# Kernel optimization log

Measured on AMD Instinct MI355X. Metric: run time of the kernel, lower is better.

Reference implementation:

```python
import jax, jax.numpy as jnp
import numpy as np

N_NODES = 50000


def setup_inputs() -> dict:
    key = jax.random.key(0)
    ks = jax.random.split(key, 6)
    L, d = 3, 128
    x = jax.random.normal(ks[0], (N_NODES, d), dtype=jnp.float32)
    edge_index = jax.random.randint(ks[1], (2, 640000), 0, N_NODES, dtype=jnp.int64)
    s = 1.0 / np.sqrt(d)
    W1 = jax.random.normal(ks[2], (L, d, d), dtype=jnp.float32) * s
    W2 = jax.random.normal(ks[3], (L, d, d), dtype=jnp.float32) * s
    b1 = jnp.zeros((L, d), dtype=jnp.float32)
    b2 = jnp.zeros((L, d), dtype=jnp.float32)
    eps = jnp.zeros((L,), dtype=jnp.float32)
    final_w = jax.random.normal(ks[4], (d + L * d, d), dtype=jnp.float32) / np.sqrt(d + L * d)
    final_b = jnp.zeros((d,), dtype=jnp.float32)
    return {"x": x, "edge_index": edge_index, "W1": W1, "b1": b1,
            "W2": W2, "b2": b2, "eps": eps, "final_w": final_w, "final_b": final_b}


def reference(x, edge_index, W1, b1, W2, b2, eps, final_w, final_b):
    src, dst = edge_index[0], edge_index[1]
    num_layers = W1.shape[0]
    xs = [x]
    h = x
    for l in range(num_layers):
        # GINConv: sum-aggregate neighbor features, add (1+eps)*self, then 2-layer MLP
        agg = jax.ops.segment_sum(h[src], dst, num_segments=N_NODES)  # [N, d]
        z = (1.0 + eps[l]) * h + agg
        z = jax.nn.relu(z @ W1[l] + b1[l])
        h = jax.nn.relu(z @ W2[l] + b2[l])
        xs.append(h)
    out = jnp.concatenate(xs, axis=-1)  # [N, in + L*out]
    return out @ final_w + final_b
```

## Files before the change

### kernel.cpp

```cpp
#include <hip/hip_runtime.h>

#define NNODES 50000
#define NEDGES 640000
#define D 128

typedef unsigned short u16;
typedef unsigned int u32;
typedef __bf16 bf16x8 __attribute__((ext_vector_type(8)));
typedef float f32x4 __attribute__((ext_vector_type(4)));
union AB { uint4 u4; bf16x8 f; };

__device__ __forceinline__ u16 f2b(float f) {
    u32 u = __float_as_uint(f);
    return (u16)((u + 0x7fffu + ((u >> 16) & 1u)) >> 16);
}
__device__ __forceinline__ u32 pack2(float lo, float hi) {
    return (u32)f2b(lo) | ((u32)f2b(hi) << 16);
}
__device__ __forceinline__ float blo(u32 v) { return __uint_as_float(v << 16); }
__device__ __forceinline__ float bhi(u32 v) { return __uint_as_float(v & 0xffff0000u); }

__device__ __forceinline__ void acc8(float* a, uint4 v) {
    a[0] += blo(v.x); a[1] += bhi(v.x);
    a[2] += blo(v.y); a[3] += bhi(v.y);
    a[4] += blo(v.z); a[5] += bhi(v.z);
    a[6] += blo(v.w); a[7] += bhi(v.w);
}


__global__ void k_hist(const int* __restrict__ dst, int* __restrict__ cnt) {
    int e = blockIdx.x * 256 + threadIdx.x;
    if (e < NEDGES) atomicAdd(&cnt[dst[e]], 1);
}

__global__ void k_scan1(const int* __restrict__ cnt, int* __restrict__ rp,
                        int* __restrict__ bsum) {
    __shared__ int s[256];
    int tid = threadIdx.x;
    int i = blockIdx.x * 256 + tid;
    int v = (i < NNODES) ? cnt[i] : 0;
    s[tid] = v;
    __syncthreads();
    for (int off = 1; off < 256; off <<= 1) {
        int t = (tid >= off) ? s[tid - off] : 0;
        __syncthreads();
        s[tid] += t;
        __syncthreads();
    }
    if (i < NNODES) rp[i] = s[tid] - v;
    if (tid == 255) bsum[blockIdx.x] = s[255];
}

__global__ void k_scan2(int* __restrict__ bsum, int nb) {
    __shared__ int s[256];
    int tid = threadIdx.x;
    int v = (tid < nb) ? bsum[tid] : 0;
    s[tid] = v;
    __syncthreads();
    for (int off = 1; off < 256; off <<= 1) {
        int t = (tid >= off) ? s[tid - off] : 0;
        __syncthreads();
        s[tid] += t;
        __syncthreads();
    }
    if (tid < nb) bsum[tid] = s[tid] - v;
}

__global__ void k_add(int* __restrict__ rp, const int* __restrict__ bsum) {
    int i = blockIdx.x * 256 + threadIdx.x;
    if (i < NNODES) rp[i] += bsum[blockIdx.x];
    if (i == 0) rp[NNODES] = NEDGES;
}

__global__ void k_scatter(const int* __restrict__ src, const int* __restrict__ dst,
                          const int* __restrict__ rp, int* __restrict__ cnt,
                          int* __restrict__ srcs) {
    int e = blockIdx.x * 256 + threadIdx.x;
    if (e < NEDGES) {
        int dn = dst[e];
        int old = atomicSub(&cnt[dn], 1);
        srcs[rp[dn] + old - 1] = src[e];
    }
}

__global__ void k_prep(const float* __restrict__ W1, const float* __restrict__ W2,
                       const float* __restrict__ fw, const float* __restrict__ x,
                       u16* __restrict__ wT1, u16* __restrict__ wT2,
                       u16* __restrict__ fwTc, u32* __restrict__ xb) {
    int idx = blockIdx.x * 256 + threadIdx.x;
    if (idx < 3 * 16384) {
        int l = idx >> 14, r = idx & 16383, n = r >> 7, k = r & 127;
        wT1[idx] = f2b(W1[l * 16384 + k * 128 + n]);
        wT2[idx] = f2b(W2[l * 16384 + k * 128 + n]);
    }
    if (idx < 4 * 16384) {
        int ch = idx >> 14, r = idx & 16383, n = r >> 7, k = r & 127;
        fwTc[idx] = f2b(fw[(ch * 128 + k) * 128 + n]);
    }
    if (idx < NNODES * 64) {
        float2 v = ((const float2*)x)[idx];
        xb[idx] = pack2(v.x, v.y);
    }
}

__global__ void k_agg(const uint4* __restrict__ h4, const int* __restrict__ rp,
                      const int* __restrict__ srcs, const float* __restrict__ epsp,
                      uint4* __restrict__ z4) {
    int tid = threadIdx.x;
    int c = tid & 15;
    int node = (blockIdx.x * 256 + tid) >> 4;
    int gbase = tid & 48;
    float sc = 1.0f + epsp[0];

    uint4 sv = h4[node * 16 + c];
    float acc[8];
    acc[0] = sc * blo(sv.x); acc[1] = sc * bhi(sv.x);
    acc[2] = sc * blo(sv.y); acc[3] = sc * bhi(sv.y);
    acc[4] = sc * blo(sv.z); acc[5] = sc * bhi(sv.z);
    acc[6] = sc * blo(sv.w); acc[7] = sc * bhi(sv.w);

    int beg = rp[node], end = rp[node + 1];
    for (int base = beg; base < end; base += 16) {
        int n = end - base; if (n > 16) n = 16;
        int myidx = (base + c < end) ? srcs[base + c] : 0;
        int j = 0;
        for (; j + 8 <= n; j += 8) {
            int s0 = __shfl(myidx, gbase + j + 0, 64);
            int s1 = __shfl(myidx, gbase + j + 1, 64);
            int s2 = __shfl(myidx, gbase + j + 2, 64);
            int s3 = __shfl(myidx, gbase + j + 3, 64);
            int s4 = __shfl(myidx, gbase + j + 4, 64);
            int s5 = __shfl(myidx, gbase + j + 5, 64);
            int s6 = __shfl(myidx, gbase + j + 6, 64);
            int s7 = __shfl(myidx, gbase + j + 7, 64);
            uint4 v0 = h4[s0 * 16 + c]; uint4 v1 = h4[s1 * 16 + c];
            uint4 v2 = h4[s2 * 16 + c]; uint4 v3 = h4[s3 * 16 + c];
            uint4 v4 = h4[s4 * 16 + c]; uint4 v5 = h4[s5 * 16 + c];
            uint4 v6 = h4[s6 * 16 + c]; uint4 v7 = h4[s7 * 16 + c];
            acc8(acc, v0); acc8(acc, v1); acc8(acc, v2); acc8(acc, v3);
            acc8(acc, v4); acc8(acc, v5); acc8(acc, v6); acc8(acc, v7);
        }
        for (; j + 4 <= n; j += 4) {
            int s0 = __shfl(myidx, gbase + j + 0, 64);
            int s1 = __shfl(myidx, gbase + j + 1, 64);
            int s2 = __shfl(myidx, gbase + j + 2, 64);
            int s3 = __shfl(myidx, gbase + j + 3, 64);
            uint4 v0 = h4[s0 * 16 + c]; uint4 v1 = h4[s1 * 16 + c];
            uint4 v2 = h4[s2 * 16 + c]; uint4 v3 = h4[s3 * 16 + c];
            acc8(acc, v0); acc8(acc, v1); acc8(acc, v2); acc8(acc, v3);
        }
        for (; j < n; ++j) {
            int s0 = __shfl(myidx, gbase + j, 64);
            uint4 v0 = h4[s0 * 16 + c];
            acc8(acc, v0);
        }
    }

    uint4 o;
    o.x = pack2(acc[0], acc[1]); o.y = pack2(acc[2], acc[3]);
    o.z = pack2(acc[4], acc[5]); o.w = pack2(acc[6], acc[7]);
    z4[node * 16 + c] = o;
}

__launch_bounds__(256, 2)
__global__ void k_mlp(const u16* __restrict__ A, const u16* __restrict__ wT1g,
                      const float* __restrict__ b1, const u16* __restrict__ wT2g,
                      const float* __restrict__ b2, u16* __restrict__ H) {
    __shared__ u16 Tb[128 * 128];
    __shared__ u16 wbuf[128 * 128];
    uint4* Tb4 = (uint4*)Tb;
    uint4* wb4 = (uint4*)wbuf;
    int tid = threadIdx.x;
    int r0 = blockIdx.x * 128;
    int wave = tid >> 6, lane = tid & 63, l16 = lane & 15, quad = lane >> 4;

    {
        const uint4* g = (const uint4*)wT1g;
        for (int i = tid; i < 2048; i += 256) {
            int n = i >> 4, ch = i & 15;
            wb4[n * 16 + ((ch + n) & 15)] = g[i];
        }
    }

    AB a[2][4];
#pragma unroll
    for (int s = 0; s < 2; ++s) {
        int row = r0 + wave * 32 + s * 16 + l16;
#pragma unroll
        for (int kb = 0; kb < 4; ++kb) {
            if (row < NNODES)
                a[s][kb].u4 = *(const uint4*)&A[row * 128 + kb * 32 + quad * 8];
            else
                a[s][kb].u4 = make_uint4(0, 0, 0, 0);
        }
    }
    __syncthreads();

    f32x4 acc[2][8];
#pragma unroll
    for (int col = 0; col < 8; ++col) {
        float bv = b1[col * 16 + l16];
        acc[0][col] = (f32x4){bv, bv, bv, bv};
        acc[1][col] = (f32x4){bv, bv, bv, bv};
    }
#pragma unroll
    for (int col = 0; col < 8; ++col) {
#pragma unroll
        for (int kb = 0; kb < 4; ++kb) {
            AB b;
            int n = col * 16 + l16;
            b.u4 = wb4[n * 16 + ((kb * 4 + quad + n) & 15)];
            acc[0][col] = __builtin_amdgcn_mfma_f32_16x16x32_bf16(a[0][kb].f, b.f, acc[0][col], 0, 0, 0);
            acc[1][col] = __builtin_amdgcn_mfma_f32_16x16x32_bf16(a[1][kb].f, b.f, acc[1][col], 0, 0, 0);
        }
    }

#pragma unroll
    for (int s = 0; s < 2; ++s)
#pragma unroll
        for (int col = 0; col < 8; ++col)
#pragma unroll
            for (int r = 0; r < 4; ++r) {
                int row = wave * 32 + s * 16 + quad * 4 + r;
                int kcol = col * 16 + l16;
                int ch = kcol >> 3;
                Tb[row * 128 + ((ch + row) & 15) * 8 + (kcol & 7)] =
                    f2b(fmaxf(acc[s][col][r], 0.f));
            }
    __syncthreads();

    {
        const uint4* g = (const uint4*)wT2g;
        for (int i = tid; i < 2048; i += 256) {
            int n = i >> 4, ch = i & 15;
            wb4[n * 16 + ((ch + n) & 15)] = g[i];
        }
    }
    AB a2[2][4];
#pragma unroll
    for (int s = 0; s < 2; ++s) {
        int m = wave * 32 + s * 16 + l16;
#pragma unroll
        for (int kb = 0; kb < 4; ++kb)
            a2[s][kb].u4 = Tb4[m * 16 + ((kb * 4 + quad + m) & 15)];
    }
    __syncthreads();

#pragma unroll
    for (int col = 0; col < 8; ++col) {
        float bv = b2[col * 16 + l16];
        acc[0][col] = (f32x4){bv, bv, bv, bv};
        acc[1][col] = (f32x4){bv, bv, bv, bv};
    }
#pragma unroll
    for (int col = 0; col < 8; ++col) {
#pragma unroll
        for (int kb = 0; kb < 4; ++kb) {
            AB b;
            int n = col * 16 + l16;
            b.u4 = wb4[n * 16 + ((kb * 4 + quad + n) & 15)];
            acc[0][col] = __builtin_amdgcn_mfma_f32_16x16x32_bf16(a2[0][kb].f, b.f, acc[0][col], 0, 0, 0);
            acc[1][col] = __builtin_amdgcn_mfma_f32_16x16x32_bf16(a2[1][kb].f, b.f, acc[1][col], 0, 0, 0);
        }
    }
    __syncthreads();

#pragma unroll
    for (int s = 0; s < 2; ++s)
#pragma unroll
        for (int col = 0; col < 8; ++col)
#pragma unroll
            for (int r = 0; r < 4; ++r) {
                int row = wave * 32 + s * 16 + quad * 4 + r;
                int kcol = col * 16 + l16;
                int ch = kcol >> 3;
                Tb[row * 128 + ((ch + row) & 15) * 8 + (kcol & 7)] =
                    f2b(fmaxf(acc[s][col][r], 0.f));
            }
    __syncthreads();

    for (int i = tid; i < 2048; i += 256) {
        int r = i >> 4, ch = i & 15;
        int grow = r0 + r;
        if (grow < NNODES)
            *(uint4*)&H[grow * 128 + ch * 8] = Tb4[r * 16 + ((ch + r) & 15)];
    }
}

__launch_bounds__(256, 2)
__global__ void k_final(const u16* __restrict__ xb, const u16* __restrict__ h1,
                        const u16* __restrict__ h2b, const u16* __restrict__ h3,
                        const u16* __restrict__ fwTc, const float* __restrict__ fb,
                        float* __restrict__ out) {
    __shared__ u16 wbuf[128 * 128];
    uint4* wb4 = (uint4*)wbuf;
    int tid = threadIdx.x;
    int wave = tid >> 6, lane = tid & 63, l16 = lane & 15, quad = lane >> 4;
    int r0 = blockIdx.x * 128 + wave * 32;

    f32x4 acc[2][8];
#pragma unroll
    for (int col = 0; col < 8; ++col) {
        float bv = fb[col * 16 + l16];
        acc[0][col] = (f32x4){bv, bv, bv, bv};
        acc[1][col] = (f32x4){bv, bv, bv, bv};
    }

    const u16* chin[4] = {xb, h1, h2b, h3};
    for (int chn = 0; chn < 4; ++chn) {
        __syncthreads();
        {
            const uint4* g = (const uint4*)(fwTc + chn * 16384);
            for (int i = tid; i < 2048; i += 256) {
                int n = i >> 4, ch = i & 15;
                wb4[n * 16 + ((ch + n) & 15)] = g[i];
            }
        }
        const u16* cp = chin[chn];
        AB a[2][4];
#pragma unroll
        for (int s = 0; s < 2; ++s) {
            int row = r0 + s * 16 + l16;
#pragma unroll
            for (int kb = 0; kb < 4; ++kb) {
                if (row < NNODES)
                    a[s][kb].u4 = *(const uint4*)&cp[row * 128 + kb * 32 + quad * 8];
                else
                    a[s][kb].u4 = make_uint4(0, 0, 0, 0);
            }
        }
        __syncthreads();
#pragma unroll
        for (int col = 0; col < 8; ++col) {
#pragma unroll
            for (int kb = 0; kb < 4; ++kb) {
                AB b;
                int n = col * 16 + l16;
                b.u4 = wb4[n * 16 + ((kb * 4 + quad + n) & 15)];
                acc[0][col] = __builtin_amdgcn_mfma_f32_16x16x32_bf16(a[0][kb].f, b.f, acc[0][col], 0, 0, 0);
                acc[1][col] = __builtin_amdgcn_mfma_f32_16x16x32_bf16(a[1][kb].f, b.f, acc[1][col], 0, 0, 0);
            }
        }
    }

#pragma unroll
    for (int s = 0; s < 2; ++s)
#pragma unroll
        for (int col = 0; col < 8; ++col)
#pragma unroll
            for (int r = 0; r < 4; ++r) {
                int row = r0 + s * 16 + quad * 4 + r;
                if (row < NNODES) out[row * 128 + col * 16 + l16] = acc[s][col][r];
            }
}

extern "C" void kernel_launch(void* const* d_in, const int* in_sizes, int n_in,
                              void* d_out, int out_size, void* d_ws, size_t ws_size,
                              hipStream_t stream) {
    const float* x   = (const float*)d_in[0];
    const int*   ei  = (const int*)d_in[1];
    const float* W1  = (const float*)d_in[2];
    const float* b1  = (const float*)d_in[3];
    const float* W2  = (const float*)d_in[4];
    const float* b2  = (const float*)d_in[5];
    const float* eps = (const float*)d_in[6];
    const float* fw  = (const float*)d_in[7];
    const float* fb  = (const float*)d_in[8];
    float* out = (float*)d_out;

    const int* srcA = ei;
    const int* dstA = ei + NEDGES;

    char* p = (char*)d_ws;
    size_t off = 0;
    auto take = [&](size_t bytes) {
        char* r = p + off;
        off = (off + bytes + 255) & ~(size_t)255;
        return r;
    };
    int* rp   = (int*)take((NNODES + 1) * sizeof(int));
    int* cnt  = (int*)take(NNODES * sizeof(int));
    int* bsum = (int*)take(256 * sizeof(int));
    int* srcs = (int*)take(NEDGES * sizeof(int));
    u16* wT1  = (u16*)take(3 * 16384 * sizeof(u16));
    u16* wT2  = (u16*)take(3 * 16384 * sizeof(u16));
    u16* fwTc = (u16*)take(4 * 16384 * sizeof(u16));
    u16* xb   = (u16*)take((size_t)NNODES * D * sizeof(u16));
    u16* zb   = (u16*)take((size_t)NNODES * D * sizeof(u16));
    u16* hb1  = (u16*)take((size_t)NNODES * D * sizeof(u16));
    u16* hb2  = (u16*)take((size_t)NNODES * D * sizeof(u16));
    u16* hb3  = (u16*)take((size_t)NNODES * D * sizeof(u16));
    (void)ws_size; (void)in_sizes; (void)n_in; (void)out_size;

    hipMemsetAsync(cnt, 0, NNODES * sizeof(int), stream);

    int nb = (NNODES + 255) / 256;
    k_hist<<<(NEDGES + 255) / 256, 256, 0, stream>>>(dstA, cnt);
    k_scan1<<<nb, 256, 0, stream>>>(cnt, rp, bsum);
    k_scan2<<<1, 256, 0, stream>>>(bsum, nb);
    k_add<<<nb, 256, 0, stream>>>(rp, bsum);
    k_scatter<<<(NEDGES + 255) / 256, 256, 0, stream>>>(srcA, dstA, rp, cnt, srcs);
    k_prep<<<(NNODES * 64 + 255) / 256, 256, 0, stream>>>(W1, W2, fw, x, wT1, wT2, fwTc, (u32*)xb);

    const u16* hin = xb;
    u16* houts[3] = {hb1, hb2, hb3};
    int gm = (NNODES + 127) / 128;
    for (int l = 0; l < 3; ++l) {
        k_agg<<<NNODES * 16 / 256, 256, 0, stream>>>((const uint4*)hin, rp, srcs, eps + l, (uint4*)zb);
        k_mlp<<<gm, 256, 0, stream>>>(zb, wT1 + l * 16384, b1 + l * D,
                                      wT2 + l * 16384, b2 + l * D, houts[l]);
        hin = houts[l];
    }
    k_final<<<gm, 256, 0, stream>>>(xb, hb1, hb2, hb3, fwTc, fb, out);
}
```

Baseline: 300.9 us.

## Fuse neighbor aggregation into MLP kernel and fold final projection into last layer

After: 315.8 us. 5.0% more time.

```diff
diff --git a/kernel.cpp b/kernel.cpp
--- a/kernel.cpp
+++ b/kernel.cpp
@@ -103,69 +103,16 @@
     }
 }
 
-__global__ void k_agg(const uint4* __restrict__ h4, const int* __restrict__ rp,
-                      const int* __restrict__ srcs, const float* __restrict__ epsp,
-                      uint4* __restrict__ z4) {
-    int tid = threadIdx.x;
-    int c = tid & 15;
-    int node = (blockIdx.x * 256 + tid) >> 4;
-    int gbase = tid & 48;
-    float sc = 1.0f + epsp[0];
-
-    uint4 sv = h4[node * 16 + c];
-    float acc[8];
-    acc[0] = sc * blo(sv.x); acc[1] = sc * bhi(sv.x);
-    acc[2] = sc * blo(sv.y); acc[3] = sc * bhi(sv.y);
-    acc[4] = sc * blo(sv.z); acc[5] = sc * bhi(sv.z);
-    acc[6] = sc * blo(sv.w); acc[7] = sc * bhi(sv.w);
-
-    int beg = rp[node], end = rp[node + 1];
-    for (int base = beg; base < end; base += 16) {
-        int n = end - base; if (n > 16) n = 16;
-        int myidx = (base + c < end) ? srcs[base + c] : 0;
-        int j = 0;
-        for (; j + 8 <= n; j += 8) {
-            int s0 = __shfl(myidx, gbase + j + 0, 64);
-            int s1 = __shfl(myidx, gbase + j + 1, 64);
-            int s2 = __shfl(myidx, gbase + j + 2, 64);
-            int s3 = __shfl(myidx, gbase + j + 3, 64);
-            int s4 = __shfl(myidx, gbase + j + 4, 64);
-            int s5 = __shfl(myidx, gbase + j + 5, 64);
-            int s6 = __shfl(myidx, gbase + j + 6, 64);
-            int s7 = __shfl(myidx, gbase + j + 7, 64);
-            uint4 v0 = h4[s0 * 16 + c]; uint4 v1 = h4[s1 * 16 + c];
-            uint4 v2 = h4[s2 * 16 + c]; uint4 v3 = h4[s3 * 16 + c];
-            uint4 v4 = h4[s4 * 16 + c]; uint4 v5 = h4[s5 * 16 + c];
-            uint4 v6 = h4[s6 * 16 + c]; uint4 v7 = h4[s7 * 16 + c];
-            acc8(acc, v0); acc8(acc, v1); acc8(acc, v2); acc8(acc, v3);
-            acc8(acc, v4); acc8(acc, v5); acc8(acc, v6); acc8(acc, v7);
-        }
-        for (; j + 4 <= n; j += 4) {
-            int s0 = __shfl(myidx, gbase + j + 0, 64);
-            int s1 = __shfl(myidx, gbase + j + 1, 64);
-            int s2 = __shfl(myidx, gbase + j + 2, 64);
-            int s3 = __shfl(myidx, gbase + j + 3, 64);
-            uint4 v0 = h4[s0 * 16 + c]; uint4 v1 = h4[s1 * 16 + c];
-            uint4 v2 = h4[s2 * 16 + c]; uint4 v3 = h4[s3 * 16 + c];
-            acc8(acc, v0); acc8(acc, v1); acc8(acc, v2); acc8(acc, v3);
-        }
-        for (; j < n; ++j) {
-            int s0 = __shfl(myidx, gbase + j, 64);
-            uint4 v0 = h4[s0 * 16 + c];
-            acc8(acc, v0);
-        }
-    }
-
-    uint4 o;
-    o.x = pack2(acc[0], acc[1]); o.y = pack2(acc[2], acc[3]);
-    o.z = pack2(acc[4], acc[5]); o.w = pack2(acc[6], acc[7]);
-    z4[node * 16 + c] = o;
-}
-
+template <bool FINAL>
 __launch_bounds__(256, 2)
-__global__ void k_mlp(const u16* __restrict__ A, const u16* __restrict__ wT1g,
-                      const float* __restrict__ b1, const u16* __restrict__ wT2g,
-                      const float* __restrict__ b2, u16* __restrict__ H) {
+__global__ void k_layer(const uint4* __restrict__ h4, const int* __restrict__ rp,
+                        const int* __restrict__ srcs, const float* __restrict__ epsp,
+                        const u16* __restrict__ wT1g, const float* __restrict__ b1,
+                        const u16* __restrict__ wT2g, const float* __restrict__ b2,
+                        u16* __restrict__ H,
+                        const u16* __restrict__ xbg, const u16* __restrict__ h1g,
+                        const u16* __restrict__ h2g, const u16* __restrict__ fwTc,
+                        const float* __restrict__ fb, float* __restrict__ out) {
     __shared__ u16 Tb[128 * 128];
     __shared__ u16 wbuf[128 * 128];
     uint4* Tb4 = (uint4*)Tb;
@@ -182,17 +129,73 @@
         }
     }
 
+    {
+        int c = tid & 15;
+        int grp = tid >> 4;
+        int gbase = lane & 48;
+        float sc = 1.0f + epsp[0];
+        for (int p = 0; p < 8; ++p) {
+            int rloc = p * 16 + grp;
+            int node = r0 + rloc;
+            uint4 o = make_uint4(0, 0, 0, 0);
+            if (node < NNODES) {
+                uint4 sv = h4[node * 16 + c];
+                float acc[8];
+                acc[0] = sc * blo(sv.x); acc[1] = sc * bhi(sv.x);
+                acc[2] = sc * blo(sv.y); acc[3] = sc * bhi(sv.y);
+                acc[4] = sc * blo(sv.z); acc[5] = sc * bhi(sv.z);
+                acc[6] = sc * blo(sv.w); acc[7] = sc * bhi(sv.w);
+                int beg = rp[node], end = rp[node + 1];
+                for (int base = beg; base < end; base += 16) {
+                    int n = end - base; if (n > 16) n = 16;
+                    int myidx = (base + c < end) ? srcs[base + c] : 0;
+                    int j = 0;
+                    for (; j + 8 <= n; j += 8) {
+                        int s0 = __shfl(myidx, gbase + j + 0, 64);
+                        int s1 = __shfl(myidx, gbase + j + 1, 64);
+                        int s2 = __shfl(myidx, gbase + j + 2, 64);
+                        int s3 = __shfl(myidx, gbase + j + 3, 64);
+                        int s4 = __shfl(myidx, gbase + j + 4, 64);
+                        int s5 = __shfl(myidx, gbase + j + 5, 64);
+                        int s6 = __shfl(myidx, gbase + j + 6, 64);
+                        int s7 = __shfl(myidx, gbase + j + 7, 64);
+                        uint4 v0 = h4[s0 * 16 + c]; uint4 v1 = h4[s1 * 16 + c];
+                        uint4 v2 = h4[s2 * 16 + c]; uint4 v3 = h4[s3 * 16 + c];
+                        uint4 v4 = h4[s4 * 16 + c]; uint4 v5 = h4[s5 * 16 + c];
+                        uint4 v6 = h4[s6 * 16 + c]; uint4 v7 = h4[s7 * 16 + c];
+                        acc8(acc, v0); acc8(acc, v1); acc8(acc, v2); acc8(acc, v3);
+                        acc8(acc, v4); acc8(acc, v5); acc8(acc, v6); acc8(acc, v7);
+                    }
+                    for (; j + 4 <= n; j += 4) {
+                        int s0 = __shfl(myidx, gbase + j + 0, 64);
+                        int s1 = __shfl(myidx, gbase + j + 1, 64);
+                        int s2 = __shfl(myidx, gbase + j + 2, 64);
+                        int s3 = __shfl(myidx, gbase + j + 3, 64);
+                        uint4 v0 = h4[s0 * 16 + c]; uint4 v1 = h4[s1 * 16 + c];
+                        uint4 v2 = h4[s2 * 16 + c]; uint4 v3 = h4[s3 * 16 + c];
+                        acc8(acc, v0); acc8(acc, v1); acc8(acc, v2); acc8(acc, v3);
+                    }
+                    for (; j < n; ++j) {
+                        int s0 = __shfl(myidx, gbase + j, 64);
+                        uint4 v0 = h4[s0 * 16 + c];
+                        acc8(acc, v0);
+                    }
+                }
+                o.x = pack2(acc[0], acc[1]); o.y = pack2(acc[2], acc[3]);
+                o.z = pack2(acc[4], acc[5]); o.w = pack2(acc[6], acc[7]);
+            }
+            Tb4[rloc * 16 + ((c + rloc) & 15)] = o;
+        }
+    }
+    __syncthreads();
+
     AB a[2][4];
 #pragma unroll
     for (int s = 0; s < 2; ++s) {
-        int row = r0 + wave * 32 + s * 16 + l16;
-#pragma unroll
-        for (int kb = 0; kb < 4; ++kb) {
-            if (row < NNODES)
-                a[s][kb].u4 = *(const uint4*)&A[row * 128 + kb * 32 + quad * 8];
-            else
-                a[s][kb].u4 = make_uint4(0, 0, 0, 0);
-        }
+        int m = wave * 32 + s * 16 + l16;
+#pragma unroll
+        for (int kb = 0; kb < 4; ++kb)
+            a[s][kb].u4 = Tb4[m * 16 + ((kb * 4 + quad + m) & 15)];
     }
     __syncthreads();
 
@@ -263,7 +266,6 @@
             acc[1][col] = __builtin_amdgcn_mfma_f32_16x16x32_bf16(a2[1][kb].f, b.f, acc[1][col], 0, 0, 0);
         }
     }
-    __syncthreads();
 
 #pragma unroll
     for (int s = 0; s < 2; ++s)
@@ -277,81 +279,78 @@
                 Tb[row * 128 + ((ch + row) & 15) * 8 + (kcol & 7)] =
                     f2b(fmaxf(acc[s][col][r], 0.f));
             }
-    __syncthreads();
-
-    for (int i = tid; i < 2048; i += 256) {
-        int r = i >> 4, ch = i & 15;
-        int grow = r0 + r;
-        if (grow < NNODES)
-            *(uint4*)&H[grow * 128 + ch * 8] = Tb4[r * 16 + ((ch + r) & 15)];
-    }
-}
-
-__launch_bounds__(256, 2)
-__global__ void k_final(const u16* __restrict__ xb, const u16* __restrict__ h1,
-                        const u16* __restrict__ h2b, const u16* __restrict__ h3,
-                        const u16* __restrict__ fwTc, const float* __restrict__ fb,
-                        float* __restrict__ out) {
-    __shared__ u16 wbuf[128 * 128];
-    uint4* wb4 = (uint4*)wbuf;
-    int tid = threadIdx.x;
-    int wave = tid >> 6, lane = tid & 63, l16 = lane & 15, quad = lane >> 4;
-    int r0 = blockIdx.x * 128 + wave * 32;
-
-    f32x4 acc[2][8];
-#pragma unroll
-    for (int col = 0; col < 8; ++col) {
-        float bv = fb[col * 16 + l16];
-        acc[0][col] = (f32x4){bv, bv, bv, bv};
-        acc[1][col] = (f32x4){bv, bv, bv, bv};
-    }
-
-    const u16* chin[4] = {xb, h1, h2b, h3};
-    for (int chn = 0; chn < 4; ++chn) {
+
+    if constexpr (!FINAL) {
         __syncthreads();
-        {
-            const uint4* g = (const uint4*)(fwTc + chn * 16384);
-            for (int i = tid; i < 2048; i += 256) {
-                int n = i >> 4, ch = i & 15;
-                wb4[n * 16 + ((ch + n) & 15)] = g[i];
-            }
-        }
-        const u16* cp = chin[chn];
-        AB a[2][4];
-#pragma unroll
-        for (int s = 0; s < 2; ++s) {
-            int row = r0 + s * 16 + l16;
-#pragma unroll
-            for (int kb = 0; kb < 4; ++kb) {
-                if (row < NNODES)
-                    a[s][kb].u4 = *(const uint4*)&cp[row * 128 + kb * 32 + quad * 8];
-                else
-                    a[s][kb].u4 = make_uint4(0, 0, 0, 0);
-            }
-        }
-        __syncthreads();
+        for (int i = tid; i < 2048; i += 256) {
+            int r = i >> 4, ch = i & 15;
+            int grow = r0 + r;
+            if (grow < NNODES)
+                *(uint4*)&H[grow * 128 + ch * 8] = Tb4[r * 16 + ((ch + r) & 15)];
+        }
+    } else {
 #pragma unroll
         for (int col = 0; col < 8; ++col) {
-#pragma unroll
-            for (int kb = 0; kb < 4; ++kb) {
-                AB b;
-                int n = col * 16 + l16;
-                b.u4 = wb4[n * 16 + ((kb * 4 + quad + n) & 15)];
-                acc[0][col] = __builtin_amdgcn_mfma_f32_16x16x32_bf16(a[0][kb].f, b.f, acc[0][col], 0, 0, 0);
-                acc[1][col] = __builtin_amdgcn_mfma_f32_16x16x32_bf16(a[1][kb].f, b.f, acc[1][col], 0, 0, 0);
-            }
-        }
-    }
-
-#pragma unroll
-    for (int s = 0; s < 2; ++s)
-#pragma unroll
-        for (int col = 0; col < 8; ++col)
-#pragma unroll
-            for (int r = 0; r < 4; ++r) {
-                int row = r0 + s * 16 + quad * 4 + r;
-                if (row < NNODES) out[row * 128 + col * 16 + l16] = acc[s][col][r];
-            }
+            float bv = fb[col * 16 + l16];
+            acc[0][col] = (f32x4){bv, bv, bv, bv};
+            acc[1][col] = (f32x4){bv, bv, bv, bv};
+        }
+        const u16* chin[3] = {xbg, h1g, h2g};
+        for (int chn = 0; chn < 4; ++chn) {
+            __syncthreads();
+            {
+                const uint4* g = (const uint4*)(fwTc + chn * 16384);
+                for (int i = tid; i < 2048; i += 256) {
+                    int n = i >> 4, ch = i & 15;
+                    wb4[n * 16 + ((ch + n) & 15)] = g[i];
+                }
+            }
+            AB af[2][4];
+            if (chn < 3) {
+                const u16* cp = chin[chn];
+#pragma unroll
+                for (int s = 0; s < 2; ++s) {
+                    int row = r0 + wave * 32 + s * 16 + l16;
+#pragma unroll
+                    for (int kb = 0; kb < 4; ++kb) {
+                        if (row < NNODES)
+                            af[s][kb].u4 = *(const uint4*)&cp[row * 128 + kb * 32 + quad * 8];
+                        else
+                            af[s][kb].u4 = make_uint4(0, 0, 0, 0);
+                    }
+                }
+            } else {
+#pragma unroll
+                for (int s = 0; s < 2; ++s) {
+                    int m = wave * 32 + s * 16 + l16;
+#pragma unroll
+                    for (int kb = 0; kb < 4; ++kb)
+                        af[s][kb].u4 = Tb4[m * 16 + ((kb * 4 + quad + m) & 15)];
+                }
+            }
+            __syncthreads();
+#pragma unroll
+            for (int col = 0; col < 8; ++col) {
+#pragma unroll
+                for (int kb = 0; kb < 4; ++kb) {
+                    AB b;
+                    int n = col * 16 + l16;
+                    b.u4 = wb4[n * 16 + ((kb * 4 + quad + n) & 15)];
+                    acc[0][col] = __builtin_amdgcn_mfma_f32_16x16x32_bf16(af[0][kb].f, b.f, acc[0][col], 0, 0, 0);
+                    acc[1][col] = __builtin_amdgcn_mfma_f32_16x16x32_bf16(af[1][kb].f, b.f, acc[1][col], 0, 0, 0);
+                }
+            }
+        }
+#pragma unroll
+        for (int s = 0; s < 2; ++s)
+#pragma unroll
+            for (int col = 0; col < 8; ++col)
+#pragma unroll
+                for (int r = 0; r < 4; ++r) {
+                    int row = r0 + wave * 32 + s * 16 + quad * 4 + r;
+                    if (row < NNODES) out[row * 128 + col * 16 + l16] = acc[s][col][r];
+                }
+    }
 }
 
 extern "C" void kernel_launch(void* const* d_in, const int* in_sizes, int n_in,
@@ -386,10 +385,8 @@
     u16* wT2  = (u16*)take(3 * 16384 * sizeof(u16));
     u16* fwTc = (u16*)take(4 * 16384 * sizeof(u16));
     u16* xb   = (u16*)take((size_t)NNODES * D * sizeof(u16));
-    u16* zb   = (u16*)take((size_t)NNODES * D * sizeof(u16));
     u16* hb1  = (u16*)take((size_t)NNODES * D * sizeof(u16));
     u16* hb2  = (u16*)take((size_t)NNODES * D * sizeof(u16));
-    u16* hb3  = (u16*)take((size_t)NNODES * D * sizeof(u16));
     (void)ws_size; (void)in_sizes; (void)n_in; (void)out_size;
 
     hipMemsetAsync(cnt, 0, NNODES * sizeof(int), stream);
@@ -402,14 +399,15 @@
     k_scatter<<<(NEDGES + 255) / 256, 256, 0, stream>>>(srcA, dstA, rp, cnt, srcs);
     k_prep<<<(NNODES * 64 + 255) / 256, 256, 0, stream>>>(W1, W2, fw, x, wT1, wT2, fwTc, (u32*)xb);
 
-    const u16* hin = xb;
-    u16* houts[3] = {hb1, hb2, hb3};
     int gm = (NNODES + 127) / 128;
-    for (int l = 0; l < 3; ++l) {
-        k_agg<<<NNODES * 16 / 256, 256, 0, stream>>>((const uint4*)hin, rp, srcs, eps + l, (uint4*)zb);
-        k_mlp<<<gm, 256, 0, stream>>>(zb, wT1 + l * 16384, b1 + l * D,
-                                      wT2 + l * 16384, b2 + l * D, houts[l]);
-        hin = houts[l];
-    }
-    k_final<<<gm, 256, 0, stream>>>(xb, hb1, hb2, hb3, fwTc, fb, out);
-}
+    k_layer<false><<<gm, 256, 0, stream>>>((const uint4*)xb, rp, srcs, eps + 0,
+                                           wT1, b1, wT2, b2, hb1,
+                                           nullptr, nullptr, nullptr, nullptr, nullptr, nullptr);
+    k_layer<false><<<gm, 256, 0, stream>>>((const uint4*)hb1, rp, srcs, eps + 1,
+                                           wT1 + 16384, b1 + D, wT2 + 16384, b2 + D, hb2,
+                                           nullptr, nullptr, nullptr, nullptr, nullptr, nullptr);
+    k_layer<true><<<gm, 256, 0, stream>>>((const uint4*)hb2, rp, srcs, eps + 2,
+                                          wT1 + 2 * 16384, b1 + 2 * D, wT2 + 2 * 16384, b2 + 2 * D,
+                                          nullptr,
+                                          xb, hb1, hb2, fwTc, fb, out);
+}
```
